# Performance work log

Hardware: AMD Instinct MI355X
Metric: run time of the kernel (lower is better)

Reference implementation:

```python
import jax, jax.numpy as jnp
import numpy as np

B, L, D, H = 16, 1024, 768, 12
PHD = D // H  # per-head dim = 64


def setup_inputs() -> dict:
    key = jax.random.key(0)
    ks = jax.random.split(key, 6)
    s = 0.02  # small init scale (xavier-like magnitude)
    return {
        "embeddings": jax.random.normal(ks[0], (B, L, D), jnp.float32),
        "pre_w": jax.random.normal(ks[1], (D, D), jnp.float32) * s,
        "pre_b": jnp.zeros((D,), jnp.float32),
        "psfs": jax.random.normal(ks[2], (H, 2 * L - 1, PHD), jnp.float32) * s,
        "post_w": jax.random.normal(ks[3], (D, D), jnp.float32) * s,
        "post_b": jnp.zeros((D,), jnp.float32),
        "sparse_mat": jax.random.normal(ks[4], (L, L), jnp.float32) * s,
        "ln_g": jnp.ones((D,), jnp.float32),
        "ln_b": jnp.zeros((D,), jnp.float32),
    }


def _spectral_norm(W, n_iters=1, eps=1e-12):
    # torch spectral_norm: power iteration with detached u, v; sigma = u^T W v
    u = jnp.ones((W.shape[0],), W.dtype) / jnp.sqrt(jnp.asarray(W.shape[0], W.dtype))
    for _ in range(n_iters):
        v = W.T @ u
        v = v / (jnp.linalg.norm(v) + eps)
        u = W @ v
        u = u / (jnp.linalg.norm(u) + eps)
    u = jax.lax.stop_gradient(u)
    v = jax.lax.stop_gradient(v)
    sigma = u @ (W @ v)
    return W / sigma


def reference(embeddings, pre_w, pre_b, psfs, post_w, post_b, sparse_mat, ln_g, ln_b):
    # pre-projection
    x = embeddings @ pre_w.T + pre_b                       # (B, L, D)
    # zero-pad along seq to 2L-1 and split heads
    xp = jnp.pad(x, ((0, 0), (0, L - 1), (0, 0)))          # (B, 2L-1, D)
    xp = xp.reshape(B, 2 * L - 1, H, PHD).transpose(0, 2, 1, 3)  # (B, H, 2L-1, d)
    # causal PSF mask: keep first L taps, zero the rest (zeros still enter softmax, as in torch)
    causal = (jnp.arange(2 * L - 1) < L)[None, :, None]
    psf = jnp.where(causal, psfs, 0.0)                     # (H, 2L-1, d)
    psf = jax.nn.softmax(psf, axis=1)
    # 2D circular convolution via FFT over (seq, head_dim)
    conv = jnp.fft.ifftn(jnp.fft.fftn(psf, axes=(1, 2))[None] * jnp.fft.fftn(xp, axes=(2, 3)), axes=(2, 3))
    conv = jnp.real(conv)[:, :, :L, :]                     # (B, H, L, d)
    conv = jax.nn.gelu(conv, approximate=False).transpose(0, 2, 1, 3).reshape(B, L, D)
    conv_emb = conv @ post_w.T + post_b
    # sparse branch: spectrally-normalized, causal-masked dense mixing matrix
    sp = jnp.tril(_spectral_norm(sparse_mat))              # (L, L)
    sparse_emb = jnp.einsum('st,btd->bsd', sp, x)
    # dropout is identity (eval), keep_prob = 1.0; residual + LayerNorm(eps=1e-12)
    y = conv_emb + sparse_emb + embeddings
    mu = jnp.mean(y, axis=-1, keepdims=True)
    var = jnp.mean((y - mu) ** 2, axis=-1, keepdims=True)
    return (y - mu) * jax.lax.rsqrt(var + 1e-12) * ln_g + ln_b
```

## Files before the change

kernel.cpp:

```cpp
#include <hip/hip_runtime.h>
#include <math.h>

#define Bn 16
#define Ln 1024
#define Dn 768
#define Hn 12
#define PHDn 64
#define NK 33
#define NHK (Hn * NK)
#define TWOPI_64 0.09817477042468103f

typedef short s16x8 __attribute__((ext_vector_type(8)));
typedef float f32x4 __attribute__((ext_vector_type(4)));
typedef unsigned short u16x4 __attribute__((ext_vector_type(4)));

__device__ __forceinline__ unsigned short f2bf(float f) {
    unsigned int u = __float_as_uint(f);
    unsigned int r = (u + 0x7FFFu + ((u >> 16) & 1u)) >> 16;
    return (unsigned short)r;
}
__device__ __forceinline__ float bf2f(unsigned short s) {
    unsigned int u = ((unsigned int)s) << 16;
    return __uint_as_float(u);
}
__device__ __forceinline__ float2 cmul(float2 a, float2 b) {
    return make_float2(a.x * b.x - a.y * b.y, a.x * b.y + a.y * b.x);
}
__device__ __forceinline__ float2 cadd(float2 a, float2 b) { return make_float2(a.x + b.x, a.y + b.y); }
__device__ __forceinline__ float2 csub(float2 a, float2 b) { return make_float2(a.x - b.x, a.y - b.y); }
__device__ __forceinline__ unsigned int packbf(float re, float im) {
    return (unsigned int)f2bf(re) | ((unsigned int)f2bf(im) << 16);
}
__device__ __forceinline__ float2 unpackbf(unsigned int v) {
    return make_float2(bf2f((unsigned short)(v & 0xffff)), bf2f((unsigned short)(v >> 16)));
}

#define SW(j) ((j) ^ (((j) >> 2) & 12) ^ (((j) >> 6) & 3))
#define PD(j) ((j) + ((j) >> 4))

static const size_t O_P    = 0;
static const size_t O_PSFH = 786432;
static const size_t O_PART = 1376256;
static const size_t O_QH   = 1597440;
static const size_t O_X    = 1598240;
static const size_t O_XH   = 14181152;
static const size_t O_YH   = 27157280;
static const size_t O_SPE  = 40146080;
static const size_t O_V    = 52728992;
static const size_t O_UR   = 52730016;
static const size_t O_SIG  = 52731040;

__global__ __launch_bounds__(256) void k_psf_softmax(const float* __restrict__ psfs,
                                                     float* __restrict__ p,
                                                     float* __restrict__ q) {
    int he = blockIdx.x;
    int h = he >> 6, e = he & 63;
    int tid = threadIdx.x;
    float ev[4];
    float s = 0.f;
#pragma unroll
    for (int i = 0; i < 4; ++i) {
        int t = tid + 256 * i;
        float v = psfs[((size_t)h * 2047 + t) * 64 + e];
        ev[i] = expf(v);
        s += ev[i];
    }
    __shared__ float red[256];
    red[tid] = s; __syncthreads();
    for (int st = 128; st > 0; st >>= 1) {
        if (tid < st) red[tid] += red[tid + st];
        __syncthreads();
    }
    float denom = red[0] + 1023.0f;
    float inv = 1.0f / denom;
#pragma unroll
    for (int i = 0; i < 4; ++i) {
        int t = tid + 256 * i;
        p[((size_t)h * 1024 + t) * 64 + e] = ev[i] * inv;
    }
    if (tid == 0) q[he] = inv;
}

__global__ __launch_bounds__(256) void k_psf_dft(const float* __restrict__ p,
                                                 float* __restrict__ psfh) {
    int blk = blockIdx.x;
    int h = blk >> 8, tb = blk & 255;
    int t0 = tb * 4;
    int tid = threadIdx.x;
    int w = tid >> 6, lane = tid & 63;
    __shared__ float pv[4][64], cc[64], ssn[64];
    if (tid < 64) {
        float ang = TWOPI_64 * tid;
        cc[tid] = cosf(ang); ssn[tid] = sinf(ang);
    }
    pv[w][lane] = p[((size_t)h * 1024 + t0 + w) * 64 + lane];
    __syncthreads();
    if (lane < NK) {
        float re = 0.f, im = 0.f;
#pragma unroll 8
        for (int e = 0; e < 64; ++e) {
            int j = (lane * e) & 63;
            float v = pv[w][e];
            re += v * cc[j];
            im -= v * ssn[j];
        }
        size_t o = (((size_t)h * NK + lane) * 1024 + t0 + w) * 2;
        psfh[o] = re; psfh[o + 1] = im;
    }
}

__global__ __launch_bounds__(64) void k_q_dft(const float* __restrict__ q,
                                              float* __restrict__ qh) {
    int h = blockIdx.x;
    int tid = threadIdx.x;
    __shared__ float qv[64], cc[64], ssn[64];
    qv[tid] = q[h * 64 + tid];
    float ang = TWOPI_64 * tid;
    cc[tid] = cosf(ang); ssn[tid] = sinf(ang);
    __syncthreads();
    if (tid < NK) {
        float re = 0.f, im = 0.f;
        for (int e = 0; e < 64; ++e) {
            int j = (tid * e) & 63;
            re += qv[e] * cc[j];
            im -= qv[e] * ssn[j];
        }
        qh[(h * NK + tid) * 2] = re;
        qh[(h * NK + tid) * 2 + 1] = im;
    }
}

__device__ __forceinline__ void build_twiddles(float2* tw, int tid) {
#pragma unroll
    for (int it = 0; it < 2; ++it) {
        int j = tid + it * 256;
        float a = (float)j * 3.0679615757712823e-3f;
        float sv, cv;
        __sincosf(a, &sv, &cv);
        tw[j] = make_float2(cv, -sv);
    }
}

__device__ __forceinline__ void fft_pair(const float2* __restrict__ X,
                                         float2* __restrict__ Y,
                                         const float2* __restrict__ tw,
                                         int tid, int m) {
#pragma unroll
    for (int it = 0; it < 2; ++it) {
        int i = tid + it * 256;
        int r = i & (m - 1);
        int am = i - r;
        float2 w1 = tw[am];
        float2 w1b = make_float2(w1.y, -w1.x);
        float2 w2 = cmul(w1, w1);
        float2 x0 = X[SW(i)], x1 = X[SW(i + 512)], x2 = X[SW(i + 1024)], x3 = X[SW(i + 1536)];
        float2 y0 = cadd(x0, x2);
        float2 y1 = cmul(csub(x0, x2), w1);
        float2 y2 = cadd(x1, x3);
        float2 y3 = cmul(csub(x1, x3), w1b);
        int o = 4 * am + r;
        Y[SW(o)] = cadd(y0, y2);
        Y[SW(o + m)] = cadd(y1, y3);
        Y[SW(o + 2 * m)] = cmul(csub(y0, y2), w2);
        Y[SW(o + 3 * m)] = cmul(csub(y1, y3), w2);
    }
}

__global__ __launch_bounds__(256) void k_tap_fft(const float* __restrict__ psfh,
                                                 const float* __restrict__ qh,
                                                 float* __restrict__ phf) {
    __shared__ float2 A[2048], B[2048], tw[512];
    int hk = blockIdx.x, tid = threadIdx.x;
    build_twiddles(tw, tid);
    float2 qv = make_float2(qh[hk * 2], qh[hk * 2 + 1]);
    const float2* Pg = (const float2*)(psfh + (size_t)hk * 2048);
    __syncthreads();
#pragma unroll
    for (int it = 0; it < 2; ++it) {
        int i = tid + it * 256;
        float2 x0 = Pg[i], x1 = Pg[i + 512];
        float2 x2 = (i == 0) ? make_float2(0.f, 0.f) : qv;
        float2 x3 = qv;
        float2 w1 = tw[i];
        float2 w1b = make_float2(w1.y, -w1.x);
        float2 w2 = cmul(w1, w1);
        float2 y0 = cadd(x0, x2);
        float2 y1 = cmul(csub(x0, x2), w1);
        float2 y2 = cadd(x1, x3);
        float2 y3 = cmul(csub(x1, x3), w1b);
        int o = 4 * i;
        A[SW(o)] = cadd(y0, y2);
        A[SW(o + 1)] = cadd(y1, y3);
        A[SW(o + 2)] = cmul(csub(y0, y2), w2);
        A[SW(o + 3)] = cmul(csub(y1, y3), w2);
    }
    __syncthreads();
    fft_pair(A, B, tw, tid, 4);   __syncthreads();
    fft_pair(B, A, tw, tid, 16);  __syncthreads();
    fft_pair(A, B, tw, tid, 64);  __syncthreads();
    fft_pair(B, A, tw, tid, 256); __syncthreads();
    float2* out = (float2*)(phf + (size_t)hk * 4096);
#pragma unroll
    for (int it = 0; it < 4; ++it) {
        int t = tid + it * 256;
        float2 lo = A[SW(t)], hi = A[SW(t + 1024)];
        out[t] = cadd(lo, hi);
        out[t + 1024] = csub(lo, hi);
    }
}

__device__ __forceinline__ void triple_tail(float2 z0, float2 z1, float2 z2, float2 z3,
                                            float2 zz0, float2 zz1, float2 zz2, float2 zz3,
                                            float2 w2, float2 w4, float2* o) {
    float2 w2b = make_float2(w2.y, -w2.x);
    float2 a0 = cadd(z0, z2),   a2 = cmul(csub(z0, z2), w2);
    float2 b0 = cadd(z1, z3),   b2 = cmul(csub(z1, z3), w2b);
    float2 a1 = cadd(zz0, zz2), a3 = cmul(csub(zz0, zz2), w2);
    float2 b1 = cadd(zz1, zz3), b3 = cmul(csub(zz1, zz3), w2b);
    o[0] = cadd(a0, b0); o[4] = cmul(csub(a0, b0), w4);
    o[1] = cadd(a1, b1); o[5] = cmul(csub(a1, b1), w4);
    o[2] = cadd(a2, b2); o[6] = cmul(csub(a2, b2), w4);
    o[3] = cadd(a3, b3); o[7] = cmul(csub(a3, b3), w4);
}

__device__ __forceinline__ void fft_triple(const float2* x, float2 w10, float2 w11, float2* o) {
    float2 w10b = make_float2(w10.y, -w10.x), w11b = make_float2(w11.y, -w11.x);
    float2 w2 = cmul(w10, w10), w4 = cmul(w2, w2);
    float2 z0 = cadd(x[0], x[4]), z1 = cadd(x[1], x[5]);
    float2 z2 = cadd(x[2], x[6]), z3 = cadd(x[3], x[7]);
    float2 zz0 = cmul(csub(x[0], x[4]), w10);
    float2 zz1 = cmul(csub(x[1], x[5]), w11);
    float2 zz2 = cmul(csub(x[2], x[6]), w10b);
    float2 zz3 = cmul(csub(x[3], x[7]), w11b);
    triple_tail(z0, z1, z2, z3, zz0, zz1, zz2, zz3, w2, w4, o);
}

__global__ __launch_bounds__(256) void k_conv_fft(const unsigned int* __restrict__ XHb,
                                                  const float* __restrict__ PHF,
                                                  unsigned int* __restrict__ YHb) {
    __shared__ float2 S[2176], tw[512];
    int bhk = blockIdx.x, tid = threadIdx.x;
    int hk = bhk % NHK;
    build_twiddles(tw, tid);
    const unsigned int* Xg = XHb + (size_t)bhk * 1024;
    float2 x[8], o[8];
#pragma unroll
    for (int k = 0; k < 4; ++k) x[k] = unpackbf(Xg[tid + 256 * k]);
    __syncthreads();
    {
        float2 w10 = tw[tid], w11 = tw[tid + 256];
        float2 w10b = make_float2(w10.y, -w10.x), w11b = make_float2(w11.y, -w11.x);
        float2 w2 = cmul(w10, w10), w4 = cmul(w2, w2);
        float2 zz0 = cmul(x[0], w10), zz1 = cmul(x[1], w11);
        float2 zz2 = cmul(x[2], w10b), zz3 = cmul(x[3], w11b);
        triple_tail(x[0], x[1], x[2], x[3], zz0, zz1, zz2, zz3, w2, w4, o);
    }
#pragma unroll
    for (int k = 0; k < 8; ++k) S[PD(8 * tid + k)] = o[k];
    __syncthreads();
    {
        int r = tid & 7, am = tid - r;
#pragma unroll
        for (int k = 0; k < 8; ++k) x[k] = S[PD(tid + 256 * k)];
        __syncthreads();
        fft_triple(x, tw[am], tw[am + 256], o);
        int base = 8 * am + r;
#pragma unroll
        for (int k = 0; k < 8; ++k) S[PD(base + 8 * k)] = o[k];
    }
    __syncthreads();
    {
        int r = tid & 63, am = tid - r;
#pragma unroll
        for (int k = 0; k < 8; ++k) x[k] = S[PD(tid + 256 * k)];
        __syncthreads();
        fft_triple(x, tw[am], tw[am + 256], o);
        int base = 8 * am + r;
#pragma unroll
        for (int k = 0; k < 8; ++k) S[PD(base + 64 * k)] = o[k];
    }
    __syncthreads();
    const float2* P = (const float2*)(PHF + (size_t)hk * 4096);
    float2 v[8];
#pragma unroll
    for (int it = 0; it < 2; ++it) {
        int i2 = tid + 256 * it;
        float2 g0 = S[PD(i2)], g1 = S[PD(i2 + 512)], g2 = S[PD(i2 + 1024)], g3 = S[PD(i2 + 1536)];
        float2 y0 = cadd(g0, g2), y1 = csub(g0, g2);
        float2 y2 = cadd(g1, g3);
        float2 d13 = csub(g1, g3);
        float2 y3 = make_float2(d13.y, -d13.x);
        float2 F0 = cadd(y0, y2);
        float2 F1 = cadd(y1, y3);
        float2 F2 = csub(y0, y2);
        float2 F3 = csub(y1, y3);
        float2 V0 = cmul(F0, P[i2]);
        float2 V1 = cmul(F1, P[i2 + 512]);
        float2 V2 = cmul(F2, P[i2 + 1024]);
        float2 V3 = cmul(F3, P[i2 + 1536]);
        v[it]     = make_float2(V0.x, -V0.y);
        v[it + 2] = make_float2(V1.x, -V1.y);
        v[it + 4] = make_float2(V2.x, -V2.y);
        v[it + 6] = make_float2(V3.x, -V3.y);
    }
    __syncthreads();
    fft_triple(v, tw[tid], tw[tid + 256], o);
#pragma unroll
    for (int k = 0; k < 8; ++k) S[PD(8 * tid + k)] = o[k];
    __syncthreads();
    {
        int r = tid & 7, am = tid - r;
#pragma unroll
        for (int k = 0; k < 8; ++k) x[k] = S[PD(tid + 256 * k)];
        __syncthreads();
        fft_triple(x, tw[am], tw[am + 256], o);
        int base = 8 * am + r;
#pragma unroll
        for (int k = 0; k < 8; ++k) S[PD(base + 8 * k)] = o[k];
    }
    __syncthreads();
    {
        int r = tid & 63, am = tid - r;
#pragma unroll
        for (int k = 0; k < 8; ++k) x[k] = S[PD(tid + 256 * k)];
        __syncthreads();
        fft_triple(x, tw[am], tw[am + 256], o);
        int base = 8 * am + r;
#pragma unroll
        for (int k = 0; k < 8; ++k) S[PD(base + 64 * k)] = o[k];
    }
    __syncthreads();
    unsigned int* Yg = YHb + (size_t)bhk * 1024;
    const float inv_n = 1.0f / 2048.0f;
#pragma unroll
    for (int it = 0; it < 2; ++it) {
        int i2 = tid + 256 * it;
        float2 g0 = S[PD(i2)], g1 = S[PD(i2 + 512)], g2 = S[PD(i2 + 1024)], g3 = S[PD(i2 + 1536)];
        float2 s02 = cadd(g0, g2), d02 = csub(g0, g2);
        float2 s13 = cadd(g1, g3);
        float2 d13 = csub(g1, g3);
        float2 mj13 = make_float2(d13.y, -d13.x);
        float2 o0 = cadd(s02, s13);
        float2 o1 = cadd(d02, mj13);
        Yg[i2] = packbf(o0.x * inv_n, -o0.y * inv_n);
        Yg[i2 + 512] = packbf(o1.x * inv_n, -o1.y * inv_n);
    }
}

__global__ __launch_bounds__(64) void k_build_wf1(unsigned short* __restrict__ W) {
    int m = blockIdx.x;
    int d = threadIdx.x;
    float val = 0.f;
    if (m < 66) {
        int k = m >> 1, od = m & 1;
        int j = (k * d) & 63;
        float ang = TWOPI_64 * (float)j;
        val = od ? -sinf(ang) : cosf(ang);
    }
    W[m * 64 + d] = f2bf(val);
}

__global__ __launch_bounds__(64) void k_build_wi1(unsigned short* __restrict__ W) {
    int m = blockIdx.x;
    int c = threadIdx.x;
    float val = 0.f;
    if (m < 64) {
        int d = m;
        int k, od;
        float ck;
        if (c == 0)      { k = 0;  od = 0; ck = 1.f / 64.f; }
        else if (c == 1) { k = 32; od = 0; ck = 1.f / 64.f; }
        else             { k = c >> 1; od = c & 1; ck = 2.f / 64.f; }
        int j = (k * d) & 63;
        float ang = TWOPI_64 * (float)j;
        val = od ? -sinf(ang) * ck : cosf(ang) * ck;
    }
    W[m * 64 + c] = f2bf(val);
}

__device__ __forceinline__ void mfma_core64(const unsigned short* __restrict__ gA0,
                                            const unsigned short* __restrict__ gB0,
                                            int nkt,
                                            unsigned short* __restrict__ As,
                                            unsigned short* __restrict__ Bs,
                                            int tid, int lane, int wr, int wc,
                                            f32x4 acc[4][4]) {
    int r0 = tid >> 1, hs = (tid & 1) << 2;
    int wbase = r0 * 64;
    int swr = r0 & 7;
    int kg = lane >> 4, cl = lane & 15;
    int fra[8], frb[8];
#pragma unroll
    for (int kk = 0; kk < 2; ++kk)
#pragma unroll
        for (int i = 0; i < 4; ++i) {
            int ra = wr * 64 + i * 16 + cl;
            fra[kk * 4 + i] = ra * 64 + (((kk * 4 + kg) ^ (ra & 7)) << 3);
            int rb = wc * 64 + i * 16 + cl;
            frb[kk * 4 + i] = rb * 64 + (((kk * 4 + kg) ^ (rb & 7)) << 3);
        }
    s16x8 a[4], b[4];
#pragma unroll
    for (int l = 0; l < 4; ++l) {
        a[l] = *(const s16x8*)(gA0 + l * 8);
        b[l] = *(const s16x8*)(gB0 + l * 8);
    }
    for (int kt = 0; kt < nkt; ++kt) {
        __syncthreads();
#pragma unroll
        for (int l = 0; l < 4; ++l) {
            *(s16x8*)&As[wbase + (((hs + l) ^ swr) << 3)] = a[l];
            *(s16x8*)&Bs[wbase + (((hs + l) ^ swr) << 3)] = b[l];
        }
        __syncthreads();
        if (kt + 1 < nkt) {
            size_t ko = (size_t)(kt + 1) * 64;
#pragma unroll
            for (int l = 0; l < 4; ++l) {
                a[l] = *(const s16x8*)(gA0 + ko + l * 8);
                b[l] = *(const s16x8*)(gB0 + ko + l * 8);
            }
        }
#pragma unroll
        for (int kk = 0; kk < 2; ++kk) {
            s16x8 af[4], bfr[4];
#pragma unroll
            for (int i = 0; i < 4; ++i) af[i] = *(const s16x8*)&As[fra[kk * 4 + i]];
#pragma unroll
            for (int i = 0; i < 4; ++i) bfr[i] = *(const s16x8*)&Bs[frb[kk * 4 + i]];
#pragma unroll
            for (int mi = 0; mi < 4; ++mi)
#pragma unroll
                for (int ni = 0; ni < 4; ++ni)
                    acc[mi][ni] = __builtin_amdgcn_mfma_f32_16x16x32_bf16(af[mi], bfr[ni], acc[mi][ni], 0, 0, 0);
        }
    }
}

__global__ __launch_bounds__(512) void k_mfma_proj(const unsigned short* __restrict__ A,
                                                   const unsigned short* __restrict__ W,
                                                   const float* __restrict__ bias,
                                                   unsigned short* __restrict__ C) {
    const int K = Dn, N = Dn;
    int n0 = blockIdx.x * 256, m0 = blockIdx.y * 128;
    int tid = threadIdx.x;
    int lane = tid & 63, wave = tid >> 6;
    int wr = wave >> 2, wc = wave & 3;
    __shared__ __align__(16) unsigned short As[8192], Bs[16384];
    f32x4 acc[4][4] = {};
    int ra0 = tid >> 2, sa0 = (tid & 3) * 2;
    int rb0 = tid >> 1, sb0 = (tid & 1) * 4;
    const unsigned short* gA = A + (size_t)(m0 + ra0) * K + sa0 * 8;
    const unsigned short* gB = W + (size_t)(n0 + rb0) * K + sb0 * 8;
    int kg = lane >> 4, cl = lane & 15;
    int fra[8], frb[8];
#pragma unroll
    for (int kk = 0; kk < 2; ++kk)
#pragma unroll
        for (int i = 0; i < 4; ++i) {
            int ra = wr * 64 + i * 16 + cl;
            fra[kk * 4 + i] = ra * 64 + (((kk * 4 + kg) ^ (ra & 7)) << 3);
            int rb = wc * 64 + i * 16 + cl;
            frb[kk * 4 + i] = rb * 64 + (((kk * 4 + kg) ^ (rb & 7)) << 3);
        }
    s16x8 a[2], b[4];
#pragma unroll
    for (int l = 0; l < 2; ++l) a[l] = *(const s16x8*)(gA + l * 8);
#pragma unroll
    for (int l = 0; l < 4; ++l) b[l] = *(const s16x8*)(gB + l * 8);
    const int nkt = K >> 6;
    for (int kt = 0; kt < nkt; ++kt) {
        __syncthreads();
#pragma unroll
        for (int l = 0; l < 2; ++l)
            *(s16x8*)&As[ra0 * 64 + (((sa0 + l) ^ (ra0 & 7)) << 3)] = a[l];
#pragma unroll
        for (int l = 0; l < 4; ++l)
            *(s16x8*)&Bs[rb0 * 64 + (((sb0 + l) ^ (rb0 & 7)) << 3)] = b[l];
        __syncthreads();
        if (kt + 1 < nkt) {
            size_t ko = (size_t)(kt + 1) * 64;
#pragma unroll
            for (int l = 0; l < 2; ++l) a[l] = *(const s16x8*)(gA + ko + l * 8);
#pragma unroll
            for (int l = 0; l < 4; ++l) b[l] = *(const s16x8*)(gB + ko + l * 8);
        }
#pragma unroll
        for (int kk = 0; kk < 2; ++kk) {
            s16x8 af[4], bfr[4];
#pragma unroll
            for (int i = 0; i < 4; ++i) af[i] = *(const s16x8*)&As[fra[kk * 4 + i]];
#pragma unroll
            for (int i = 0; i < 4; ++i) bfr[i] = *(const s16x8*)&Bs[frb[kk * 4 + i]];
#pragma unroll
            for (int mi = 0; mi < 4; ++mi)
#pragma unroll
                for (int ni = 0; ni < 4; ++ni)
                    acc[mi][ni] = __builtin_amdgcn_mfma_f32_16x16x32_bf16(af[mi], bfr[ni], acc[mi][ni], 0, 0, 0);
        }
    }
#pragma unroll
    for (int ni = 0; ni < 4; ++ni) {
        int gn = n0 + wc * 64 + ni * 16 + cl;
        float bv = bias[gn];
#pragma unroll
        for (int mi = 0; mi < 4; ++mi) {
            int gm = m0 + wr * 64 + mi * 16 + kg * 4;
            f32x4 v = acc[mi][ni];
#pragma unroll
            for (int ri = 0; ri < 4; ++ri)
                C[(size_t)(gm + ri) * N + gn] = f2bf(v[ri] + bv);
        }
    }
}

__global__ __launch_bounds__(256) void k_mfma_dft_h(const unsigned short* __restrict__ Wf1,
                                                    const unsigned short* __restrict__ Xb,
                                                    unsigned int* __restrict__ XHb) {
    int n0 = blockIdx.x * 128;
    int h = blockIdx.y;
    int tid = threadIdx.x;
    int lane = tid & 63, wave = tid >> 6;
    int wr = wave >> 1, wc = wave & 1;
    __shared__ __align__(16) unsigned short As[8192], Bs[8192];
    f32x4 acc[4][4] = {};
    int r0 = tid >> 1, hs = (tid & 1) << 2;
    const unsigned short* gA0 = Wf1 + r0 * 64 + hs * 8;
    const unsigned short* gB0 = Xb + (size_t)(n0 + r0) * Dn + h * 64 + hs * 8;
    mfma_core64(gA0, gB0, 1, As, Bs, tid, lane, wr, wc, acc);
    int kg = lane >> 4, cl = lane & 15;
#pragma unroll
    for (int ni = 0; ni < 4; ++ni) {
        int gn = n0 + wc * 64 + ni * 16 + cl;
        int b = gn >> 10, u = gn & 1023;
#pragma unroll
        for (int mi = 0; mi < 4; ++mi) {
            int gmb = wr * 64 + mi * 16 + kg * 4;
            f32x4 v = acc[mi][ni];
#pragma unroll
            for (int rp = 0; rp < 2; ++rp) {
                int m = gmb + rp * 2;
                if (m < 66) {
                    size_t plane = (size_t)(b * Hn + h) * NK + (m >> 1);
                    XHb[plane * 1024 + u] = packbf(v[rp * 2], v[rp * 2 + 1]);
                }
            }
        }
    }
}

__global__ __launch_bounds__(256) void k_transpose_yh(const unsigned int* __restrict__ YHb,
                                                      unsigned short* __restrict__ YT) {
    int ut = blockIdx.x & 7;
    int h = (blockIdx.x >> 3) % 12;
    int b = blockIdx.x / 96;
    int u0 = ut * 128;
    __shared__ unsigned short T[128 * 66];
    int tid = threadIdx.x;
    int planeBase = (b * Hn + h) * NK;
#pragma unroll
    for (int i = 0; i < 17; ++i) {
        int idx = tid + i * 256;
        if (idx < 4224) {
            int k = idx >> 7, uo = idx & 127;
            unsigned int v = YHb[(size_t)(planeBase + k) * 1024 + u0 + uo];
            T[uo * 66 + 2 * k] = (unsigned short)(v & 0xffff);
            T[uo * 66 + 2 * k + 1] = (unsigned short)(v >> 16);
        }
    }
    __syncthreads();
    unsigned int* out = (unsigned int*)YT;
#pragma unroll
    for (int i = 0; i < 16; ++i) {
        int idx = tid + i * 256;
        int uo = idx >> 5, w = idx & 31;
        unsigned int lo, hi;
        if (w == 0) {
            lo = T[uo * 66 + 0];
            hi = T[uo * 66 + 64];
        } else {
            lo = T[uo * 66 + 2 * w];
            hi = T[uo * 66 + 2 * w + 1];
        }
        size_t r = (size_t)b * 1024 + u0 + uo;
        out[r * 384 + h * 32 + w] = lo | (hi << 16);
    }
}

__global__ __launch_bounds__(256) void k_mfma_idft_h(const unsigned short* __restrict__ YT,
                                                     const unsigned short* __restrict__ Wi1,
                                                     unsigned short* __restrict__ G) {
    int m0 = blockIdx.x * 128;
    int h = blockIdx.y;
    int tid = threadIdx.x;
    int lane = tid & 63, wave = tid >> 6;
    int wr = wave >> 1, wc = wave & 1;
    __shared__ __align__(16) unsigned short As[8192], Bs[8192];
    f32x4 acc[4][4] = {};
    int r0 = tid >> 1, hs = (tid & 1) << 2;
    const unsigned short* gA0 = YT + (size_t)(m0 + r0) * Dn + h * 64 + hs * 8;
    const unsigned short* gB0 = Wi1 + r0 * 64 + hs * 8;
    mfma_core64(gA0, gB0, 1, As, Bs, tid, lane, wr, wc, acc);
    int kg = lane >> 4, cl = lane & 15;
#pragma unroll
    for (int ni = 0; ni < 4; ++ni) {
        int gn = wc * 64 + ni * 16 + cl;
        if (gn < 64) {
#pragma unroll
            for (int mi = 0; mi < 4; ++mi) {
                int gm = m0 + wr * 64 + mi * 16 + kg * 4;
                f32x4 v = acc[mi][ni];
#pragma unroll
                for (int ri = 0; ri < 4; ++ri) {
                    float c = v[ri];
                    float g = c * 0.5f * (1.0f + erff(c * 0.70710678118f));
                    G[(size_t)(gm + ri) * Dn + h * 64 + gn] = f2bf(g);
                }
            }
        }
    }
}

__global__ __launch_bounds__(256) void k_mfma_sparse(const unsigned short* __restrict__ SP,
                                                     const unsigned short* __restrict__ XT,
                                                     const float* __restrict__ sigbuf,
                                                     unsigned short* __restrict__ C) {
    int bx = blockIdx.x;
    int mt = bx & 7, nt = (bx >> 3) % 6, b = bx / 48;
    int m0 = mt * 128, n0 = nt * 128;
    const unsigned short* Xb = XT + (size_t)b * Dn * Ln;
    unsigned short* Cb = C + (size_t)b * Ln * Dn;
    int tid = threadIdx.x;
    int lane = tid & 63, wave = tid >> 6;
    int wr = wave >> 1, wc = wave & 1;
    __shared__ __align__(16) unsigned short As[8192], Bs[8192];
    f32x4 acc[4][4] = {};
    int r0 = tid >> 1, hs = (tid & 1) << 2;
    const unsigned short* gA0 = SP + (size_t)(m0 + r0) * Ln + hs * 8;
    const unsigned short* gB0 = Xb + (size_t)(n0 + r0) * Ln + hs * 8;
    mfma_core64(gA0, gB0, 2 * mt + 2, As, Bs, tid, lane, wr, wc, acc);
    float invs = sigbuf[0];
    int kg = lane >> 4, cl = lane & 15;
#pragma unroll
    for (int ni = 0; ni < 4; ++ni) {
        int gn = n0 + wc * 64 + ni * 16 + cl;
#pragma unroll
        for (int mi = 0; mi < 4; ++mi) {
            int gm = m0 + wr * 64 + mi * 16 + kg * 4;
            f32x4 v = acc[mi][ni];
#pragma unroll
            for (int ri = 0; ri < 4; ++ri)
                Cb[(size_t)(gm + ri) * Dn + gn] = f2bf(v[ri] * invs);
        }
    }
}

__global__ __launch_bounds__(256) void k_cvt_bf16(const float* __restrict__ in,
                                                  unsigned short* __restrict__ out, int n4) {
    int i = blockIdx.x * 256 + threadIdx.x;
    if (i < n4) {
        float4 v = ((const float4*)in)[i];
        u16x4 o;
        o[0] = f2bf(v.x); o[1] = f2bf(v.y); o[2] = f2bf(v.z); o[3] = f2bf(v.w);
        *(u16x4*)&out[(size_t)i * 4] = o;
    }
}

__global__ __launch_bounds__(256) void k_cvt_sp(const float* __restrict__ SP,
                                                unsigned short* __restrict__ O) {
    int s = blockIdx.x;
    int t0 = threadIdx.x * 4;
    float4 v = *(const float4*)&SP[(size_t)s * 1024 + t0];
    u16x4 o;
    o[0] = (t0 + 0 <= s) ? f2bf(v.x) : 0;
    o[1] = (t0 + 1 <= s) ? f2bf(v.y) : 0;
    o[2] = (t0 + 2 <= s) ? f2bf(v.z) : 0;
    o[3] = (t0 + 3 <= s) ? f2bf(v.w) : 0;
    *(u16x4*)&O[(size_t)s * 1024 + t0] = o;
}

__global__ __launch_bounds__(256) void k_transpose_x(const unsigned short* __restrict__ X,
                                                     unsigned short* __restrict__ XT) {
    int d0 = blockIdx.x * 64, t0 = blockIdx.y * 64, b = blockIdx.z;
    const unsigned short* Xb = X + (size_t)b * Ln * Dn;
    unsigned short* Tb = XT + (size_t)b * Dn * Ln;
    __shared__ unsigned short tile[64 * 65];
    int tx = threadIdx.x & 63, ty = threadIdx.x >> 6;
#pragma unroll
    for (int i = 0; i < 16; ++i) {
        int t = ty + i * 4;
        tile[t * 65 + tx] = Xb[(size_t)(t0 + t) * Dn + d0 + tx];
    }
    __syncthreads();
#pragma unroll
    for (int i = 0; i < 16; ++i) {
        int d = ty + i * 4;
        Tb[(size_t)(d0 + d) * Ln + t0 + tx] = tile[tx * 65 + d];
    }
}

__global__ __launch_bounds__(256) void k_sn_colsum(const float* __restrict__ Wm,
                                                   float* __restrict__ partial) {
    int b = blockIdx.x;
    int tid = threadIdx.x;
    int c0 = tid * 4;
    float4 s = make_float4(0.f, 0.f, 0.f, 0.f);
#pragma unroll
    for (int i = 0; i < 16; ++i) {
        float4 v = *(const float4*)&Wm[(size_t)(b * 16 + i) * 1024 + c0];
        s.x += v.x; s.y += v.y; s.z += v.z; s.w += v.w;
    }
    *(float4*)&partial[(size_t)b * 1024 + c0] = s;
}

__global__ __launch_bounds__(1024) void k_sn_v2(const float* __restrict__ partial,
                                                float* __restrict__ v) {
    int j = threadIdx.x;
    float s = 0.f;
#pragma unroll 8
    for (int i = 0; i < 64; ++i) s += partial[(size_t)i * 1024 + j];
    s *= 0.03125f;
    __shared__ float red[1024];
    red[j] = s * s; __syncthreads();
    for (int st = 512; st > 0; st >>= 1) {
        if (j < st) red[j] += red[j + st];
        __syncthreads();
    }
    float nrm = sqrtf(red[0]);
    v[j] = s / (nrm + 1e-12f);
}

__global__ __launch_bounds__(64) void k_sn_u(const float* __restrict__ Wm,
                                             const float* __restrict__ v,
                                             float* __restrict__ ur) {
    int i = blockIdx.x;
    int lane = threadIdx.x;
    float s = 0.f;
    for (int j = lane; j < 1024; j += 64) s += Wm[(size_t)i * 1024 + j] * v[j];
#pragma unroll
    for (int off = 32; off > 0; off >>= 1) s += __shfl_down(s, off);
    if (lane == 0) ur[i] = s;
}

__global__ __launch_bounds__(1024) void k_sn_sigma(const float* __restrict__ ur,
                                                   float* __restrict__ sig) {
    int i = threadIdx.x;
    __shared__ float red[1024];
    float u = ur[i];
    red[i] = u * u; __syncthreads();
    for (int st = 512; st > 0; st >>= 1) {
        if (i < st) red[i] += red[i + st];
        __syncthreads();
    }
    if (i == 0) {
        float ss = red[0];
        float sigma = ss / (sqrtf(ss) + 1e-12f);
        sig[0] = 1.0f / sigma;
    }
}

__global__ __launch_bounds__(256) void k_final_ln(const unsigned short* __restrict__ CE,
                                                  const unsigned short* __restrict__ SE,
                                                  const float* __restrict__ EMB,
                                                  const float* __restrict__ g,
                                                  const float* __restrict__ be,
                                                  float* __restrict__ out) {
    int r = blockIdx.x;
    int tid = threadIdx.x;
    float y[3];
    float s = 0.f;
#pragma unroll
    for (int i = 0; i < 3; ++i) {
        int o = tid + i * 256;
        size_t idx = (size_t)r * 768 + o;
        y[i] = bf2f(CE[idx]) + bf2f(SE[idx]) + EMB[idx];
        s += y[i];
    }
    __shared__ float red[256];
    red[tid] = s; __syncthreads();
    for (int st = 128; st > 0; st >>= 1) {
        if (tid < st) red[tid] += red[tid + st];
        __syncthreads();
    }
    float mu = red[0] * (1.f / 768.f);
    __syncthreads();
    float vs = 0.f;
#pragma unroll
    for (int i = 0; i < 3; ++i) { float d = y[i] - mu; vs += d * d; }
    red[tid] = vs; __syncthreads();
    for (int st = 128; st > 0; st >>= 1) {
        if (tid < st) red[tid] += red[tid + st];
        __syncthreads();
    }
    float var = red[0] * (1.f / 768.f);
    float rstd = rsqrtf(var + 1e-12f);
#pragma unroll
    for (int i = 0; i < 3; ++i) {
        int o = tid + i * 256;
        size_t idx = (size_t)r * 768 + o;
        out[idx] = (y[i] - mu) * rstd * g[o] + be[o];
    }
}

extern "C" void kernel_launch(void* const* d_in, const int* in_sizes, int n_in,
                              void* d_out, int out_size, void* d_ws, size_t ws_size,
                              hipStream_t stream) {
    const float* emb     = (const float*)d_in[0];
    const float* pre_w   = (const float*)d_in[1];
    const float* pre_b   = (const float*)d_in[2];
    const float* psfs    = (const float*)d_in[3];
    const float* post_w  = (const float*)d_in[4];
    const float* post_b  = (const float*)d_in[5];
    const float* spmat   = (const float*)d_in[6];
    const float* ln_g    = (const float*)d_in[7];
    const float* ln_b    = (const float*)d_in[8];
    float* out = (float*)d_out;
    float* ws = (float*)d_ws;

    float* p      = ws + O_P;
    float* psfh   = ws + O_PSFH;
    float* part   = ws + O_PART;
    float* qh     = ws + O_QH;
    float* q      = ws + O_SIG + 8;
    unsigned int* XHb = (unsigned int*)(ws + O_XH);
    unsigned int* YHb = (unsigned int*)(ws + O_YH);
    float* phf    = ws + O_SPE;
    float* v      = ws + O_V;
    float* urw    = ws + O_UR;
    float* sig    = ws + O_SIG;

    unsigned short* x_bf      = (unsigned short*)(ws + O_X);
    unsigned short* Wf1       = (unsigned short*)(ws + O_X + 6291456);
    unsigned short* Wi1       = (unsigned short*)(ws + O_X + 6295552);
    unsigned short* YT        = (unsigned short*)(ws + O_XH);
    unsigned short* xT_bf     = (unsigned short*)(ws + O_XH);
    unsigned short* emb_bf    = (unsigned short*)(ws + O_YH);
    unsigned short* CE_bf     = (unsigned short*)(ws + O_YH);
    unsigned short* spe_bf    = (unsigned short*)(ws + O_SPE);
    unsigned short* G_bf      = (unsigned short*)(ws + O_SPE + 3145728);
    unsigned short* SP_bf     = (unsigned short*)(ws + O_P);
    unsigned short* pre_w_bf  = (unsigned short*)(ws + O_PSFH);
    unsigned short* post_w_bf = (unsigned short*)(ws + O_PSFH + 294912);

    k_psf_softmax<<<Hn * 64, 256, 0, stream>>>(psfs, p, q);
    k_psf_dft<<<Hn * 256, 256, 0, stream>>>(p, psfh);
    k_q_dft<<<Hn, 64, 0, stream>>>(q, qh);
    k_tap_fft<<<NHK, 256, 0, stream>>>(psfh, qh, phf);

    k_sn_colsum<<<64, 256, 0, stream>>>(spmat, part);
    k_sn_v2<<<1, 1024, 0, stream>>>(part, v);
    k_sn_u<<<1024, 64, 0, stream>>>(spmat, v, urw);
    k_sn_sigma<<<1, 1024, 0, stream>>>(urw, sig);

    k_cvt_sp<<<1024, 256, 0, stream>>>(spmat, SP_bf);
    k_cvt_bf16<<<576, 256, 0, stream>>>(pre_w, pre_w_bf, 147456);
    k_cvt_bf16<<<576, 256, 0, stream>>>(post_w, post_w_bf, 147456);
    k_cvt_bf16<<<12288, 256, 0, stream>>>(emb, emb_bf, 3145728);
    k_build_wf1<<<128, 64, 0, stream>>>(Wf1);
    k_build_wi1<<<128, 64, 0, stream>>>(Wi1);

    k_mfma_proj<<<dim3(3, 128), 512, 0, stream>>>(emb_bf, pre_w_bf, pre_b, x_bf);

    k_mfma_dft_h<<<dim3(128, Hn), 256, 0, stream>>>(Wf1, x_bf, XHb);

    k_conv_fft<<<Bn * NHK, 256, 0, stream>>>(XHb, phf, YHb);

    k_transpose_yh<<<Bn * Hn * 8, 256, 0, stream>>>(YHb, YT);

    k_mfma_idft_h<<<dim3(128, Hn), 256, 0, stream>>>(YT, Wi1, G_bf);

    k_transpose_x<<<dim3(12, 16, Bn), 256, 0, stream>>>(x_bf, xT_bf);

    k_mfma_proj<<<dim3(3, 128), 512, 0, stream>>>(G_bf, post_w_bf, post_b, CE_bf);

    k_mfma_sparse<<<768, 256, 0, stream>>>(SP_bf, xT_bf, sig, spe_bf);

    k_final_ln<<<Bn * Ln, 256, 0, stream>>>(CE_bf, spe_bf, emb, ln_g, ln_b, out);
}
```

Before: 310.9 us.

## Fuse YH transpose into inverse-DFT GEMM and read bf16 embeddings in LayerNorm

Removes the separate k_transpose_yh kernel: the inverse-DFT MFMA kernel now gathers its A tile straight from the packed YH planes into swizzled shared memory, skipping a global write and reread of the transposed tensor. The final LayerNorm now reads the bf16 embedding copy instead of the fp32 original, halving that read, at some precision cost in the residual term. Workspace buffers are remapped so emb_bf stays live until the end and does not overlap YH or CE.

```diff
diff --git a/kernel.cpp b/kernel.cpp
--- a/kernel.cpp
+++ b/kernel.cpp
@@ -549,14 +549,16 @@
     }
 }
 
-__global__ __launch_bounds__(256) void k_transpose_yh(const unsigned int* __restrict__ YHb,
-                                                      unsigned short* __restrict__ YT) {
-    int ut = blockIdx.x & 7;
-    int h = (blockIdx.x >> 3) % 12;
-    int b = blockIdx.x / 96;
-    int u0 = ut * 128;
-    __shared__ unsigned short T[128 * 66];
+__global__ __launch_bounds__(256) void k_mfma_idft_h(const unsigned int* __restrict__ YHb,
+                                                     const unsigned short* __restrict__ Wi1,
+                                                     unsigned short* __restrict__ G) {
+    int m0 = blockIdx.x * 128;
+    int h = blockIdx.y;
+    int b = m0 >> 10, u0 = m0 & 1023;
     int tid = threadIdx.x;
+    int lane = tid & 63, wave = tid >> 6;
+    int wr = wave >> 1, wc = wave & 1;
+    __shared__ __align__(16) unsigned short As[8192], Bs[8192];
     int planeBase = (b * Hn + h) * NK;
 #pragma unroll
     for (int i = 0; i < 17; ++i) {
@@ -564,44 +566,48 @@
         if (idx < 4224) {
             int k = idx >> 7, uo = idx & 127;
             unsigned int v = YHb[(size_t)(planeBase + k) * 1024 + u0 + uo];
-            T[uo * 66 + 2 * k] = (unsigned short)(v & 0xffff);
-            T[uo * 66 + 2 * k + 1] = (unsigned short)(v >> 16);
-        }
-    }
-    __syncthreads();
-    unsigned int* out = (unsigned int*)YT;
-#pragma unroll
-    for (int i = 0; i < 16; ++i) {
-        int idx = tid + i * 256;
-        int uo = idx >> 5, w = idx & 31;
-        unsigned int lo, hi;
-        if (w == 0) {
-            lo = T[uo * 66 + 0];
-            hi = T[uo * 66 + 64];
-        } else {
-            lo = T[uo * 66 + 2 * w];
-            hi = T[uo * 66 + 2 * w + 1];
-        }
-        size_t r = (size_t)b * 1024 + u0 + uo;
-        out[r * 384 + h * 32 + w] = lo | (hi << 16);
-    }
-}
-
-__global__ __launch_bounds__(256) void k_mfma_idft_h(const unsigned short* __restrict__ YT,
-                                                     const unsigned short* __restrict__ Wi1,
-                                                     unsigned short* __restrict__ G) {
-    int m0 = blockIdx.x * 128;
-    int h = blockIdx.y;
-    int tid = threadIdx.x;
-    int lane = tid & 63, wave = tid >> 6;
-    int wr = wave >> 1, wc = wave & 1;
-    __shared__ __align__(16) unsigned short As[8192], Bs[8192];
+            unsigned short lo = (unsigned short)(v & 0xffff);
+            unsigned short hi = (unsigned short)(v >> 16);
+            int sw = uo & 7;
+            int rb = uo * 64;
+            if (k == 0) {
+                As[rb + (sw << 3) + 0] = lo;
+            } else if (k == 32) {
+                As[rb + (sw << 3) + 1] = lo;
+            } else {
+                int c0 = 2 * k, c1 = 2 * k + 1;
+                As[rb + (((c0 >> 3) ^ sw) << 3) + (c0 & 7)] = lo;
+                As[rb + (((c1 >> 3) ^ sw) << 3) + (c1 & 7)] = hi;
+            }
+        }
+    }
+    {
+        int r0 = tid >> 1, hs = (tid & 1) << 2;
+        int swr = r0 & 7;
+        const unsigned short* gB0 = Wi1 + r0 * 64 + hs * 8;
+#pragma unroll
+        for (int l = 0; l < 4; ++l)
+            *(s16x8*)&Bs[r0 * 64 + (((hs + l) ^ swr) << 3)] = *(const s16x8*)(gB0 + l * 8);
+    }
+    __syncthreads();
     f32x4 acc[4][4] = {};
-    int r0 = tid >> 1, hs = (tid & 1) << 2;
-    const unsigned short* gA0 = YT + (size_t)(m0 + r0) * Dn + h * 64 + hs * 8;
-    const unsigned short* gB0 = Wi1 + r0 * 64 + hs * 8;
-    mfma_core64(gA0, gB0, 1, As, Bs, tid, lane, wr, wc, acc);
     int kg = lane >> 4, cl = lane & 15;
+#pragma unroll
+    for (int kk = 0; kk < 2; ++kk) {
+        s16x8 af[4], bfr[4];
+#pragma unroll
+        for (int i = 0; i < 4; ++i) {
+            int ra = wr * 64 + i * 16 + cl;
+            af[i] = *(const s16x8*)&As[ra * 64 + (((kk * 4 + kg) ^ (ra & 7)) << 3)];
+            int rbw = wc * 64 + i * 16 + cl;
+            bfr[i] = *(const s16x8*)&Bs[rbw * 64 + (((kk * 4 + kg) ^ (rbw & 7)) << 3)];
+        }
+#pragma unroll
+        for (int mi = 0; mi < 4; ++mi)
+#pragma unroll
+            for (int ni = 0; ni < 4; ++ni)
+                acc[mi][ni] = __builtin_amdgcn_mfma_f32_16x16x32_bf16(af[mi], bfr[ni], acc[mi][ni], 0, 0, 0);
+    }
 #pragma unroll
     for (int ni = 0; ni < 4; ++ni) {
         int gn = wc * 64 + ni * 16 + cl;
@@ -761,7 +767,7 @@
 
 __global__ __launch_bounds__(256) void k_final_ln(const unsigned short* __restrict__ CE,
                                                   const unsigned short* __restrict__ SE,
-                                                  const float* __restrict__ EMB,
+                                                  const unsigned short* __restrict__ EMB,
                                                   const float* __restrict__ g,
                                                   const float* __restrict__ be,
                                                   float* __restrict__ out) {
@@ -773,7 +779,7 @@
     for (int i = 0; i < 3; ++i) {
         int o = tid + i * 256;
         size_t idx = (size_t)r * 768 + o;
-        y[i] = bf2f(CE[idx]) + bf2f(SE[idx]) + EMB[idx];
+        y[i] = bf2f(CE[idx]) + bf2f(SE[idx]) + bf2f(EMB[idx]);
         s += y[i];
     }
     __shared__ float red[256];
@@ -822,20 +828,19 @@
     float* part   = ws + O_PART;
     float* qh     = ws + O_QH;
     float* q      = ws + O_SIG + 8;
-    unsigned int* XHb = (unsigned int*)(ws + O_XH);
-    unsigned int* YHb = (unsigned int*)(ws + O_YH);
     float* phf    = ws + O_SPE;
     float* v      = ws + O_V;
     float* urw    = ws + O_UR;
     float* sig    = ws + O_SIG;
 
+    unsigned int* XHb = (unsigned int*)(ws + O_XH);
+    unsigned int* YHb = (unsigned int*)(ws + O_YH + 6291456);
+    unsigned short* emb_bf    = (unsigned short*)(ws + O_YH);
     unsigned short* x_bf      = (unsigned short*)(ws + O_X);
     unsigned short* Wf1       = (unsigned short*)(ws + O_X + 6291456);
     unsigned short* Wi1       = (unsigned short*)(ws + O_X + 6295552);
-    unsigned short* YT        = (unsigned short*)(ws + O_XH);
     unsigned short* xT_bf     = (unsigned short*)(ws + O_XH);
-    unsigned short* emb_bf    = (unsigned short*)(ws + O_YH);
-    unsigned short* CE_bf     = (unsigned short*)(ws + O_YH);
+    unsigned short* CE_bf     = (unsigned short*)(ws + O_XH + 6488064);
     unsigned short* spe_bf    = (unsigned short*)(ws + O_SPE);
     unsigned short* G_bf      = (unsigned short*)(ws + O_SPE + 3145728);
     unsigned short* SP_bf     = (unsigned short*)(ws + O_P);
@@ -865,9 +870,7 @@
 
     k_conv_fft<<<Bn * NHK, 256, 0, stream>>>(XHb, phf, YHb);
 
-    k_transpose_yh<<<Bn * Hn * 8, 256, 0, stream>>>(YHb, YT);
-
-    k_mfma_idft_h<<<dim3(128, Hn), 256, 0, stream>>>(YT, Wi1, G_bf);
+    k_mfma_idft_h<<<dim3(128, Hn), 256, 0, stream>>>(YHb, Wi1, G_bf);
 
     k_transpose_x<<<dim3(12, 16, Bn), 256, 0, stream>>>(x_bf, xT_bf);
 
@@ -875,5 +878,5 @@
 
     k_mfma_sparse<<<768, 256, 0, stream>>>(SP_bf, xT_bf, sig, spe_bf);
 
-    k_final_ln<<<Bn * Ln, 256, 0, stream>>>(CE_bf, spe_bf, emb, ln_g, ln_b, out);
-}
+    k_final_ln<<<Bn * Ln, 256, 0, stream>>>(CE_bf, spe_bf, emb_bf, ln_g, ln_b, out);
+}
```

New measurement: 304.6 us. 1.02x faster.
